# Performance work log

Hardware: AMD Instinct MI355X
Metric: run time of the kernel (lower is better)

Reference implementation:

```python
import jax, jax.numpy as jnp
import numpy as np

N_NODES = 50000
N_EDGES = 800000
D_MODEL = 128
N_HEADS = 8
HEAD_DIM = D_MODEL // N_HEADS
EPS = 1e-5


def setup_inputs() -> dict:
    key = jax.random.key(0)
    ks = jax.random.split(key, 8)
    return {
        "node_feature": jax.random.normal(ks[0], (N_NODES, D_MODEL), jnp.float32),
        "dist_attn": jax.random.normal(ks[1], (N_EDGES, N_HEADS), jnp.float32),
        "path_attn": jax.random.normal(ks[2], (N_EDGES, N_HEADS), jnp.float32),
        "gamma": jnp.ones((D_MODEL,), jnp.float32),
        "beta": jnp.zeros((D_MODEL,), jnp.float32),
        "W_qkv": jax.random.normal(ks[3], (3 * D_MODEL, D_MODEL), jnp.float32) * (D_MODEL ** -0.5),
        "b_qkv": jnp.zeros((3 * D_MODEL,), jnp.float32),
        "W_out": jax.random.normal(ks[4], (D_MODEL, D_MODEL), jnp.float32) * (D_MODEL ** -0.5),
        "b_out": jnp.zeros((D_MODEL,), jnp.float32),
        "src": jax.random.randint(ks[5], (N_EDGES,), 0, N_NODES, jnp.int32),
        "dst": jax.random.randint(ks[6], (N_EDGES,), 0, N_NODES, jnp.int32),
    }


def reference(node_feature, dist_attn, path_attn, gamma, beta,
              W_qkv, b_qkv, W_out, b_out, src, dst):
    res = node_feature
    # LayerNorm
    mu = jnp.mean(node_feature, axis=-1, keepdims=True)
    var = jnp.var(node_feature, axis=-1, keepdims=True)
    x = (node_feature - mu) * jax.lax.rsqrt(var + EPS) * gamma + beta
    # QKV projection; scale = d_model**-0.5 (as in source, full d_model)
    qkv = (x @ W_qkv.T + b_qkv).reshape(-1, 3, N_HEADS, HEAD_DIM)
    q = qkv[:, 0] * (D_MODEL ** -0.5)  # [N, H, Dh]
    k = qkv[:, 1]
    v = qkv[:, 2]
    # u_dot_v: dot of src Q with dst K per edge/head -> [E, H]
    node_attn = jnp.einsum("ehd,ehd->eh", q[src], k[dst])
    a = node_attn + dist_attn + path_attn  # [E, H]
    # edge_softmax: segmented softmax over incoming edges of each dst node
    m = jax.ops.segment_max(a, dst, num_segments=N_NODES)  # [N, H]
    ex = jnp.exp(a - m[dst])
    denom = jax.ops.segment_sum(ex, dst, num_segments=N_NODES)  # [N, H]
    sa = ex / denom[dst]  # [E, H]
    # weighted message from src v, summed into dst
    he = v[src] * sa[:, :, None]  # [E, H, Dh]
    agg = jax.ops.segment_sum(he, dst, num_segments=N_NODES)  # [N, H, Dh]
    agg = agg.reshape(-1, D_MODEL)
    out = res + (agg @ W_out.T + b_out)
    return out
```

## Files before the change

kernel.cpp:

```cpp
#include <hip/hip_runtime.h>
#include <math.h>

#define N_NODES 50000
#define N_EDGES 800000
#define D 128
#define NH 8
#define EPS 1e-5f
#define QSCALE 0.08838834764831845f

#define TQ 24
#define TO 8

typedef __attribute__((ext_vector_type(8))) short short8;
typedef __attribute__((ext_vector_type(4))) float f32x4;

__device__ __forceinline__ unsigned short f2bf_rne(float f) {
    unsigned int u = __float_as_uint(f);
    u += 0x7fff + ((u >> 16) & 1);
    return (unsigned short)(u >> 16);
}
__device__ __forceinline__ float bf2f(unsigned short h) {
    return __uint_as_float(((unsigned int)h) << 16);
}
__device__ __forceinline__ float2 bfpair(unsigned int u) {
    return make_float2(__uint_as_float(u << 16),
                       __uint_as_float(u & 0xffff0000u));
}

__device__ __forceinline__ void gload_lds16(const void* g, void* l) {
    __builtin_amdgcn_global_load_lds(
        (const __attribute__((address_space(1))) unsigned int*)g,
        (__attribute__((address_space(3))) unsigned int*)l, 16, 0, 0);
}

__device__ __forceinline__ float qdot(uint4 u, float4 kv) {
    float2 q0 = bfpair(u.x), q1 = bfpair(u.z);
    return q0.x * kv.x + q0.y * kv.y + q1.x * kv.z + q1.y * kv.w;
}
__device__ __forceinline__ void vacc(uint4 u, float w, float& sden,
                                     float& a0, float& a1, float& a2, float& a3) {
    float2 v0 = bfpair(u.y), v1 = bfpair(u.w);
    sden += w;
    a0 += w * v0.x; a1 += w * v0.y; a2 += w * v1.x; a3 += w * v1.y;
}

__global__ void k_prep(const float* __restrict__ Wqkv, const float* __restrict__ Wout,
                       unsigned short* __restrict__ wq_t, unsigned short* __restrict__ wo_t,
                       int* __restrict__ cnt) {
    const int i = blockIdx.x * blockDim.x + threadIdx.x;
    if (i < N_NODES) cnt[i] = 0;
    if (i < TQ * 256) {
        const int nt = i >> 8, r = (i >> 4) & 15, c8 = i & 15;
        const float* s = Wqkv + (size_t)(nt * 16 + r) * D + c8 * 8;
        short8 h8, l8;
        #pragma unroll
        for (int j = 0; j < 8; j++) {
            float w = s[j];
            unsigned short h = f2bf_rne(w);
            h8[j] = (short)h;
            l8[j] = (short)f2bf_rne(w - bf2f(h));
        }
        const int off = (r * 256 + c8 * 16) ^ ((r & 7) << 4);
        char* base = (char*)wq_t + (size_t)nt * 8192;
        *(short8*)(base + off)        = h8;
        *(short8*)(base + 4096 + off) = l8;
    }
    if (i < TO * 256) {
        const int nt = i >> 8, r = (i >> 4) & 15, c8 = i & 15;
        const float* s = Wout + (size_t)(nt * 16 + r) * D + c8 * 8;
        short8 h8, l8;
        #pragma unroll
        for (int j = 0; j < 8; j++) {
            float w = s[j];
            unsigned short h = f2bf_rne(w);
            h8[j] = (short)h;
            l8[j] = (short)f2bf_rne(w - bf2f(h));
        }
        const int off = (r * 256 + c8 * 16) ^ ((r & 7) << 4);
        char* base = (char*)wo_t + (size_t)nt * 8192;
        *(short8*)(base + off)        = h8;
        *(short8*)(base + 4096 + off) = l8;
    }
}

__global__ void k_hist(const int* __restrict__ dst, int* __restrict__ cnt,
                       int* __restrict__ rank) {
    const int e0 = (blockIdx.x * blockDim.x + threadIdx.x) * 4;
    if (e0 >= N_EDGES) return;
    const int4 d4 = *(const int4*)(dst + e0);
    int r0 = atomicAdd(&cnt[d4.x], 1);
    int r1 = atomicAdd(&cnt[d4.y], 1);
    int r2 = atomicAdd(&cnt[d4.z], 1);
    int r3 = atomicAdd(&cnt[d4.w], 1);
    *(int4*)(rank + e0) = make_int4(r0, r1, r2, r3);
}

#define SCB 1024
#define SCG ((N_NODES + SCB - 1) / SCB)

__global__ void k_scan1(const int* __restrict__ cnt, int* __restrict__ row_start,
                        int* __restrict__ bsum) {
    __shared__ int wsum[16];
    const int tid = threadIdx.x, lane = tid & 63, wid = tid >> 6;
    const int gid = blockIdx.x * SCB + tid;
    const int v = (gid < N_NODES) ? cnt[gid] : 0;

    int x = v;
    #pragma unroll
    for (int off = 1; off < 64; off <<= 1) {
        int t = __shfl_up(x, off);
        if (lane >= off) x += t;
    }
    if (lane == 63) wsum[wid] = x;
    __syncthreads();
    if (wid == 0) {
        int w = (lane < 16) ? wsum[lane] : 0;
        #pragma unroll
        for (int off = 1; off < 16; off <<= 1) {
            int t = __shfl_up(w, off);
            if (lane >= off) w += t;
        }
        if (lane < 16) wsum[lane] = w;
    }
    __syncthreads();
    const int base = (wid > 0) ? wsum[wid - 1] : 0;
    const int incl = base + x;
    if (gid < N_NODES) row_start[gid] = incl - v;
    if (tid == SCB - 1) bsum[blockIdx.x] = incl;
}

__global__ void k_scan2(const int* __restrict__ bsum, int* __restrict__ row_start) {
    __shared__ int boff_s;
    const int tid = threadIdx.x;
    if (tid < 64) {
        int v = (tid < blockIdx.x) ? bsum[tid] : 0;
        #pragma unroll
        for (int off = 1; off < 64; off <<= 1) v += __shfl_xor(v, off);
        if (tid == 0) boff_s = v;
    }
    __syncthreads();
    const int gid = blockIdx.x * SCB + tid;
    if (gid < N_NODES) row_start[gid] += boff_s;
    if (gid == 0) row_start[N_NODES] = N_EDGES;
}

__global__ void k_fill(const int* __restrict__ src, const int* __restrict__ dst,
                       const int* __restrict__ rank, const int* __restrict__ row_start,
                       const float* __restrict__ dist, const float* __restrict__ path,
                       int* __restrict__ ssrc, unsigned short* __restrict__ dp16) {
    const int e0 = (blockIdx.x * blockDim.x + threadIdx.x) * 4;
    if (e0 >= N_EDGES) return;
    const int4 s4 = *(const int4*)(src + e0);
    const int4 d4 = *(const int4*)(dst + e0);
    const int4 r4 = *(const int4*)(rank + e0);
    int p0 = row_start[d4.x] + r4.x;
    int p1 = row_start[d4.y] + r4.y;
    int p2 = row_start[d4.z] + r4.z;
    int p3 = row_start[d4.w] + r4.w;

    const int ss[4] = {s4.x, s4.y, s4.z, s4.w};
    const int pp[4] = {p0, p1, p2, p3};
    #pragma unroll
    for (int j = 0; j < 4; j++) {
        const int e = e0 + j;
        float4 da = *(const float4*)(dist + (size_t)e * 8);
        float4 db = *(const float4*)(dist + (size_t)e * 8 + 4);
        float4 pa = *(const float4*)(path + (size_t)e * 8);
        float4 pb = *(const float4*)(path + (size_t)e * 8 + 4);
        short8 w;
        w[0] = (short)f2bf_rne(da.x + pa.x);
        w[1] = (short)f2bf_rne(da.y + pa.y);
        w[2] = (short)f2bf_rne(da.z + pa.z);
        w[3] = (short)f2bf_rne(da.w + pa.w);
        w[4] = (short)f2bf_rne(db.x + pb.x);
        w[5] = (short)f2bf_rne(db.y + pb.y);
        w[6] = (short)f2bf_rne(db.z + pb.z);
        w[7] = (short)f2bf_rne(db.w + pb.w);
        ssrc[pp[j]] = ss[j];
        *(short8*)(dp16 + (size_t)pp[j] * 8) = w;
    }
}

__launch_bounds__(256)
__global__ void k_ln_qkv(const float* __restrict__ nf, const float* __restrict__ gamma,
                         const float* __restrict__ beta,
                         const unsigned short* __restrict__ wq_t,
                         const float* __restrict__ bqkv,
                         unsigned short* __restrict__ qv, float* __restrict__ kb) {
    __shared__ __align__(16) char lds[2][8192];
    const int lane  = threadIdx.x & 63;
    const int wv    = threadIdx.x >> 6;
    const int nbase = blockIdx.x * 64 + wv * 16;
    const int mrow  = lane & 15;
    const int kg    = lane >> 4;

    int gn = nbase + mrow;
    if (gn >= N_NODES) gn = N_NODES - 1;
    const float* xrow = nf + (size_t)gn * D + kg * 8;
    float4 xa[4], xb[4];
    #pragma unroll
    for (int t = 0; t < 4; t++) {
        xa[t] = *(const float4*)(xrow + t * 32);
        xb[t] = *(const float4*)(xrow + t * 32 + 4);
    }
    float s = 0.f, ss = 0.f;
    #pragma unroll
    for (int t = 0; t < 4; t++) {
        s  += xa[t].x + xa[t].y + xa[t].z + xa[t].w
            + xb[t].x + xb[t].y + xb[t].z + xb[t].w;
        ss += xa[t].x * xa[t].x + xa[t].y * xa[t].y + xa[t].z * xa[t].z + xa[t].w * xa[t].w
            + xb[t].x * xb[t].x + xb[t].y * xb[t].y + xb[t].z * xb[t].z + xb[t].w * xb[t].w;
    }
    s += __shfl_xor(s, 16); ss += __shfl_xor(ss, 16);
    s += __shfl_xor(s, 32); ss += __shfl_xor(ss, 32);
    float mu   = s * (1.f / 128.f);
    float var  = ss * (1.f / 128.f) - mu * mu;
    float rstd = rsqrtf(var + EPS);

    short8 ahi[4], alo[4];
    #pragma unroll
    for (int t = 0; t < 4; t++) {
        const float* gp = gamma + kg * 8 + t * 32;
        const float* bp = beta  + kg * 8 + t * 32;
        float4 g0 = *(const float4*)gp, g1 = *(const float4*)(gp + 4);
        float4 b0 = *(const float4*)bp, b1 = *(const float4*)(bp + 4);
        float xn[8];
        xn[0] = (xa[t].x - mu) * rstd * g0.x + b0.x;
        xn[1] = (xa[t].y - mu) * rstd * g0.y + b0.y;
        xn[2] = (xa[t].z - mu) * rstd * g0.z + b0.z;
        xn[3] = (xa[t].w - mu) * rstd * g0.w + b0.w;
        xn[4] = (xb[t].x - mu) * rstd * g1.x + b1.x;
        xn[5] = (xb[t].y - mu) * rstd * g1.y + b1.y;
        xn[6] = (xb[t].z - mu) * rstd * g1.z + b1.z;
        xn[7] = (xb[t].w - mu) * rstd * g1.w + b1.w;
        #pragma unroll
        for (int j = 0; j < 8; j++) {
            unsigned short h = f2bf_rne(xn[j]);
            ahi[t][j] = (short)h;
            alo[t][j] = (short)f2bf_rne(xn[j] - bf2f(h));
        }
    }

    int boff[4];
    #pragma unroll
    for (int t = 0; t < 4; t++)
        boff[t] = (mrow * 256 + (kg + 4 * t) * 16) ^ ((mrow & 7) << 4);

    {
        const char* g0 = (const char*)wq_t + (size_t)0 * 8192 + wv * 2048 + lane * 16;
        gload_lds16(g0,        lds[0] + wv * 2048);
        gload_lds16(g0 + 1024, lds[0] + wv * 2048 + 1024);
    }
    __syncthreads();

    int cur = 0;
    for (int nt = 0; nt < TQ; ++nt) {
        if (nt + 1 < TQ) {
            const char* g0 = (const char*)wq_t + (size_t)(nt + 1) * 8192 + wv * 2048 + lane * 16;
            gload_lds16(g0,        lds[cur ^ 1] + wv * 2048);
            gload_lds16(g0 + 1024, lds[cur ^ 1] + wv * 2048 + 1024);
        }

        f32x4 acc0 = {0.f, 0.f, 0.f, 0.f};
        f32x4 acc1 = {0.f, 0.f, 0.f, 0.f};
        #pragma unroll
        for (int t = 0; t < 4; t++) {
            short8 bh = *(const short8*)(lds[cur] + boff[t]);
            short8 bl = *(const short8*)(lds[cur] + 4096 + boff[t]);
            acc0 = __builtin_amdgcn_mfma_f32_16x16x32_bf16(ahi[t], bh, acc0, 0, 0, 0);
            acc1 = __builtin_amdgcn_mfma_f32_16x16x32_bf16(alo[t], bh, acc1, 0, 0, 0);
            acc0 = __builtin_amdgcn_mfma_f32_16x16x32_bf16(ahi[t], bl, acc0, 0, 0, 0);
        }

        const int col = nt * 16 + mrow;
        if (nt < 8) {
            float bias = bqkv[col];
            #pragma unroll
            for (int r = 0; r < 4; r++) {
                int node = nbase + kg * 4 + r;
                unsigned int hq = f2bf_rne((acc0[r] + acc1[r] + bias) * QSCALE);
                unsigned int ph = __shfl_xor((int)hq, 1);
                if (!(mrow & 1) && node < N_NODES) {
                    unsigned int u2 = (hq & 0xffffu) | (ph << 16);
                    *(unsigned int*)(qv + (size_t)node * 256 + ((col >> 1) << 2)) = u2;
                }
            }
        } else if (nt < 16) {
            float bias = bqkv[col];
            #pragma unroll
            for (int r = 0; r < 4; r++) {
                int node = nbase + kg * 4 + r;
                if (node < N_NODES)
                    kb[(size_t)node * D + (col - 128)] = acc0[r] + acc1[r] + bias;
            }
        } else {
            float bias = bqkv[col];
            #pragma unroll
            for (int r = 0; r < 4; r++) {
                int node = nbase + kg * 4 + r;
                unsigned int hq = f2bf_rne(acc0[r] + acc1[r] + bias);
                unsigned int ph = __shfl_xor((int)hq, 1);
                if (!(mrow & 1) && node < N_NODES) {
                    unsigned int u2 = (hq & 0xffffu) | (ph << 16);
                    int cv = col - 256;
                    *(unsigned int*)(qv + (size_t)node * 256 + ((cv >> 1) << 2) + 2) = u2;
                }
            }
        }

        __syncthreads();
        cur ^= 1;
    }
}

__launch_bounds__(256, 4)
__global__ void k_gather(const unsigned short* __restrict__ qv,
                         const float* __restrict__ kb,
                         const unsigned short* __restrict__ dp16,
                         const int* __restrict__ row_start,
                         const int* __restrict__ ssrc,
                         float* __restrict__ agg) {
    const int node = blockIdx.x * 4 + (threadIdx.x >> 6);
    if (node >= N_NODES) return;
    const int lane = threadIdx.x & 63;
    const int half = lane >> 5;
    const int l    = lane & 31;
    const int h    = l >> 2;
    const int beg = row_start[node], end = row_start[node + 1];

    const float4 kv = *(const float4*)(kb + (size_t)node * D + 4 * l);
    float sden = 0.f, a0 = 0.f, a1 = 0.f, a2 = 0.f, a3 = 0.f;

    int i = beg + half;
    for (; i + 6 < end; i += 8) {
        int s0 = ssrc[i], s1 = ssrc[i + 2], s2 = ssrc[i + 4], s3 = ssrc[i + 6];
        uint4 u0 = *(const uint4*)(qv + (size_t)s0 * 256 + l * 8);
        uint4 u1 = *(const uint4*)(qv + (size_t)s1 * 256 + l * 8);
        uint4 u2 = *(const uint4*)(qv + (size_t)s2 * 256 + l * 8);
        uint4 u3 = *(const uint4*)(qv + (size_t)s3 * 256 + l * 8);
        float d0 = bf2f(dp16[(size_t)i * 8 + h]);
        float d1 = bf2f(dp16[(size_t)(i + 2) * 8 + h]);
        float d2 = bf2f(dp16[(size_t)(i + 4) * 8 + h]);
        float d3 = bf2f(dp16[(size_t)(i + 6) * 8 + h]);

        float p0 = qdot(u0, kv), p1 = qdot(u1, kv);
        float p2 = qdot(u2, kv), p3 = qdot(u3, kv);
        p0 += __shfl_xor(p0, 1); p1 += __shfl_xor(p1, 1);
        p2 += __shfl_xor(p2, 1); p3 += __shfl_xor(p3, 1);
        p0 += __shfl_xor(p0, 2); p1 += __shfl_xor(p1, 2);
        p2 += __shfl_xor(p2, 2); p3 += __shfl_xor(p3, 2);

        float w0 = __expf(p0 + d0), w1 = __expf(p1 + d1);
        float w2 = __expf(p2 + d2), w3 = __expf(p3 + d3);
        vacc(u0, w0, sden, a0, a1, a2, a3);
        vacc(u1, w1, sden, a0, a1, a2, a3);
        vacc(u2, w2, sden, a0, a1, a2, a3);
        vacc(u3, w3, sden, a0, a1, a2, a3);
    }
    if (i + 2 < end) {
        int s0 = ssrc[i], s1 = ssrc[i + 2];
        uint4 u0 = *(const uint4*)(qv + (size_t)s0 * 256 + l * 8);
        uint4 u1 = *(const uint4*)(qv + (size_t)s1 * 256 + l * 8);
        float d0 = bf2f(dp16[(size_t)i * 8 + h]);
        float d1 = bf2f(dp16[(size_t)(i + 2) * 8 + h]);
        float p0 = qdot(u0, kv), p1 = qdot(u1, kv);
        p0 += __shfl_xor(p0, 1); p1 += __shfl_xor(p1, 1);
        p0 += __shfl_xor(p0, 2); p1 += __shfl_xor(p1, 2);
        float w0 = __expf(p0 + d0), w1 = __expf(p1 + d1);
        vacc(u0, w0, sden, a0, a1, a2, a3);
        vacc(u1, w1, sden, a0, a1, a2, a3);
        i += 4;
    }
    if (i < end) {
        int s0 = ssrc[i];
        uint4 u0 = *(const uint4*)(qv + (size_t)s0 * 256 + l * 8);
        float d0 = bf2f(dp16[(size_t)i * 8 + h]);
        float p0 = qdot(u0, kv);
        p0 += __shfl_xor(p0, 1); p0 += __shfl_xor(p0, 2);
        float w0 = __expf(p0 + d0);
        vacc(u0, w0, sden, a0, a1, a2, a3);
    }

    sden += __shfl_xor(sden, 32);
    a0 += __shfl_xor(a0, 32);
    a1 += __shfl_xor(a1, 32);
    a2 += __shfl_xor(a2, 32);
    a3 += __shfl_xor(a3, 32);

    const float inv = (end > beg) ? 1.f / sden : 0.f;
    if (half == 0) {
        float4 r = make_float4(a0 * inv, a1 * inv, a2 * inv, a3 * inv);
        *(float4*)(agg + (size_t)node * D + 4 * l) = r;
    }
}

__launch_bounds__(256)
__global__ void k_out(const float* __restrict__ agg,
                      const unsigned short* __restrict__ wo_t,
                      const float* __restrict__ bout, const float* __restrict__ nf,
                      float* __restrict__ out) {
    __shared__ __align__(16) char lds[2][8192];
    const int lane  = threadIdx.x & 63;
    const int wv    = threadIdx.x >> 6;
    const int nbase = blockIdx.x * 64 + wv * 16;
    const int mrow  = lane & 15;
    const int kg    = lane >> 4;

    int gn = nbase + mrow;
    if (gn >= N_NODES) gn = N_NODES - 1;
    const float* arow = agg + (size_t)gn * D + kg * 8;

    short8 ahi[4], alo[4];
    #pragma unroll
    for (int t = 0; t < 4; t++) {
        float4 x0 = *(const float4*)(arow + t * 32);
        float4 x1 = *(const float4*)(arow + t * 32 + 4);
        float xn[8] = {x0.x, x0.y, x0.z, x0.w, x1.x, x1.y, x1.z, x1.w};
        #pragma unroll
        for (int j = 0; j < 8; j++) {
            unsigned short h = f2bf_rne(xn[j]);
            ahi[t][j] = (short)h;
            alo[t][j] = (short)f2bf_rne(xn[j] - bf2f(h));
        }
    }

    int boff[4];
    #pragma unroll
    for (int t = 0; t < 4; t++)
        boff[t] = (mrow * 256 + (kg + 4 * t) * 16) ^ ((mrow & 7) << 4);

    {
        const char* g0 = (const char*)wo_t + (size_t)0 * 8192 + wv * 2048 + lane * 16;
        gload_lds16(g0,        lds[0] + wv * 2048);
        gload_lds16(g0 + 1024, lds[0] + wv * 2048 + 1024);
    }
    __syncthreads();

    int cur = 0;
    for (int nt = 0; nt < TO; ++nt) {
        if (nt + 1 < TO) {
            const char* g0 = (const char*)wo_t + (size_t)(nt + 1) * 8192 + wv * 2048 + lane * 16;
            gload_lds16(g0,        lds[cur ^ 1] + wv * 2048);
            gload_lds16(g0 + 1024, lds[cur ^ 1] + wv * 2048 + 1024);
        }

        f32x4 acc0 = {0.f, 0.f, 0.f, 0.f};
        f32x4 acc1 = {0.f, 0.f, 0.f, 0.f};
        #pragma unroll
        for (int t = 0; t < 4; t++) {
            short8 bh = *(const short8*)(lds[cur] + boff[t]);
            short8 bl = *(const short8*)(lds[cur] + 4096 + boff[t]);
            acc0 = __builtin_amdgcn_mfma_f32_16x16x32_bf16(ahi[t], bh, acc0, 0, 0, 0);
            acc1 = __builtin_amdgcn_mfma_f32_16x16x32_bf16(alo[t], bh, acc1, 0, 0, 0);
            acc0 = __builtin_amdgcn_mfma_f32_16x16x32_bf16(ahi[t], bl, acc0, 0, 0, 0);
        }

        const int col = nt * 16 + mrow;
        float bias = bout[col];
        #pragma unroll
        for (int r = 0; r < 4; r++) {
            int node = nbase + kg * 4 + r;
            if (node < N_NODES)
                out[(size_t)node * D + col] =
                    nf[(size_t)node * D + col] + bias + acc0[r] + acc1[r];
        }

        __syncthreads();
        cur ^= 1;
    }
}

extern "C" void kernel_launch(void* const* d_in, const int* in_sizes, int n_in,
                              void* d_out, int out_size, void* d_ws, size_t ws_size,
                              hipStream_t stream) {
    const float* nf    = (const float*)d_in[0];
    const float* dist  = (const float*)d_in[1];
    const float* path  = (const float*)d_in[2];
    const float* gamma = (const float*)d_in[3];
    const float* beta  = (const float*)d_in[4];
    const float* Wqkv  = (const float*)d_in[5];
    const float* bqkv  = (const float*)d_in[6];
    const float* Wout  = (const float*)d_in[7];
    const float* bout  = (const float*)d_in[8];
    const int*   src   = (const int*)d_in[9];
    const int*   dst   = (const int*)d_in[10];
    float* out = (float*)d_out;

    float* kb  = (float*)d_ws;
    float* agg = kb + (size_t)N_NODES * D;
    unsigned short* qvb  = (unsigned short*)(agg + (size_t)N_NODES * D);
    unsigned short* dp16 = qvb + (size_t)N_NODES * 256;
    int* ssrc      = (int*)(dp16 + (size_t)N_EDGES * 8);
    int* rank      = ssrc + N_EDGES;
    int* cnt       = rank + N_EDGES;
    int* row_start = cnt + N_NODES;
    int* bsum      = row_start + N_NODES + 1;
    uintptr_t p = (uintptr_t)(bsum + 64);
    p = (p + 15) & ~(uintptr_t)15;
    unsigned short* wq_t = (unsigned short*)p;
    unsigned short* wo_t = wq_t + TQ * 4096;

    (void)in_sizes; (void)n_in; (void)out_size; (void)ws_size;

    hipLaunchKernelGGL(k_prep, dim3((N_NODES + 255) / 256), dim3(256), 0, stream,
                       Wqkv, Wout, wq_t, wo_t, cnt);

    hipLaunchKernelGGL(k_hist, dim3((N_EDGES / 4 + 255) / 256), dim3(256), 0, stream,
                       dst, cnt, rank);
    hipLaunchKernelGGL(k_scan1, dim3(SCG), dim3(SCB), 0, stream,
                       cnt, row_start, bsum);
    hipLaunchKernelGGL(k_scan2, dim3(SCG), dim3(SCB), 0, stream,
                       bsum, row_start);
    hipLaunchKernelGGL(k_fill, dim3((N_EDGES / 4 + 255) / 256), dim3(256), 0, stream,
                       src, dst, rank, row_start, dist, path, ssrc, dp16);

    hipLaunchKernelGGL(k_ln_qkv, dim3((N_NODES + 63) / 64), dim3(256), 0, stream,
                       nf, gamma, beta, wq_t, bqkv, qvb, kb);

    hipLaunchKernelGGL(k_gather, dim3((N_NODES + 3) / 4), dim3(256), 0, stream,
                       qvb, kb, dp16, row_start, ssrc, agg);

    hipLaunchKernelGGL(k_out, dim3((N_NODES + 63) / 64), dim3(256), 0, stream,
                       agg, wo_t, bout, nf, out);
}
```

Baseline: 204.2 us.

## Precombine dist+path in hist pass and store K as bf16

The bf16 conversion of dist+path moves from the scatter kernel into the histogram kernel, which now writes it in edge order. The fill kernel then only copies 16-byte packed rows to their CSR positions instead of reading 64 bytes of fp32 per edge at scatter time. K is stored as bf16 instead of fp32, halving its footprint and its read in the gather kernel. This adds an extra intermediate buffer with a write and read, and the lower K precision may cost accuracy.

```diff
diff --git a/kernel.cpp b/kernel.cpp
--- a/kernel.cpp
+++ b/kernel.cpp
@@ -83,8 +83,10 @@
     }
 }
 
-__global__ void k_hist(const int* __restrict__ dst, int* __restrict__ cnt,
-                       int* __restrict__ rank) {
+__global__ void k_hist(const int* __restrict__ dst,
+                       const float* __restrict__ dist, const float* __restrict__ path,
+                       int* __restrict__ cnt, int* __restrict__ rank,
+                       unsigned short* __restrict__ dps) {
     const int e0 = (blockIdx.x * blockDim.x + threadIdx.x) * 4;
     if (e0 >= N_EDGES) return;
     const int4 d4 = *(const int4*)(dst + e0);
@@ -92,74 +94,6 @@
     int r1 = atomicAdd(&cnt[d4.y], 1);
     int r2 = atomicAdd(&cnt[d4.z], 1);
     int r3 = atomicAdd(&cnt[d4.w], 1);
-    *(int4*)(rank + e0) = make_int4(r0, r1, r2, r3);
-}
-
-#define SCB 1024
-#define SCG ((N_NODES + SCB - 1) / SCB)
-
-__global__ void k_scan1(const int* __restrict__ cnt, int* __restrict__ row_start,
-                        int* __restrict__ bsum) {
-    __shared__ int wsum[16];
-    const int tid = threadIdx.x, lane = tid & 63, wid = tid >> 6;
-    const int gid = blockIdx.x * SCB + tid;
-    const int v = (gid < N_NODES) ? cnt[gid] : 0;
-
-    int x = v;
-    #pragma unroll
-    for (int off = 1; off < 64; off <<= 1) {
-        int t = __shfl_up(x, off);
-        if (lane >= off) x += t;
-    }
-    if (lane == 63) wsum[wid] = x;
-    __syncthreads();
-    if (wid == 0) {
-        int w = (lane < 16) ? wsum[lane] : 0;
-        #pragma unroll
-        for (int off = 1; off < 16; off <<= 1) {
-            int t = __shfl_up(w, off);
-            if (lane >= off) w += t;
-        }
-        if (lane < 16) wsum[lane] = w;
-    }
-    __syncthreads();
-    const int base = (wid > 0) ? wsum[wid - 1] : 0;
-    const int incl = base + x;
-    if (gid < N_NODES) row_start[gid] = incl - v;
-    if (tid == SCB - 1) bsum[blockIdx.x] = incl;
-}
-
-__global__ void k_scan2(const int* __restrict__ bsum, int* __restrict__ row_start) {
-    __shared__ int boff_s;
-    const int tid = threadIdx.x;
-    if (tid < 64) {
-        int v = (tid < blockIdx.x) ? bsum[tid] : 0;
-        #pragma unroll
-        for (int off = 1; off < 64; off <<= 1) v += __shfl_xor(v, off);
-        if (tid == 0) boff_s = v;
-    }
-    __syncthreads();
-    const int gid = blockIdx.x * SCB + tid;
-    if (gid < N_NODES) row_start[gid] += boff_s;
-    if (gid == 0) row_start[N_NODES] = N_EDGES;
-}
-
-__global__ void k_fill(const int* __restrict__ src, const int* __restrict__ dst,
-                       const int* __restrict__ rank, const int* __restrict__ row_start,
-                       const float* __restrict__ dist, const float* __restrict__ path,
-                       int* __restrict__ ssrc, unsigned short* __restrict__ dp16) {
-    const int e0 = (blockIdx.x * blockDim.x + threadIdx.x) * 4;
-    if (e0 >= N_EDGES) return;
-    const int4 s4 = *(const int4*)(src + e0);
-    const int4 d4 = *(const int4*)(dst + e0);
-    const int4 r4 = *(const int4*)(rank + e0);
-    int p0 = row_start[d4.x] + r4.x;
-    int p1 = row_start[d4.y] + r4.y;
-    int p2 = row_start[d4.z] + r4.z;
-    int p3 = row_start[d4.w] + r4.w;
-
-    const int ss[4] = {s4.x, s4.y, s4.z, s4.w};
-    const int pp[4] = {p0, p1, p2, p3};
     #pragma unroll
     for (int j = 0; j < 4; j++) {
         const int e = e0 + j;
@@ -176,9 +110,82 @@
         w[5] = (short)f2bf_rne(db.y + pb.y);
         w[6] = (short)f2bf_rne(db.z + pb.z);
         w[7] = (short)f2bf_rne(db.w + pb.w);
-        ssrc[pp[j]] = ss[j];
-        *(short8*)(dp16 + (size_t)pp[j] * 8) = w;
-    }
+        *(short8*)(dps + (size_t)e * 8) = w;
+    }
+    *(int4*)(rank + e0) = make_int4(r0, r1, r2, r3);
+}
+
+#define SCB 1024
+#define SCG ((N_NODES + SCB - 1) / SCB)
+
+__global__ void k_scan1(const int* __restrict__ cnt, int* __restrict__ row_start,
+                        int* __restrict__ bsum) {
+    __shared__ int wsum[16];
+    const int tid = threadIdx.x, lane = tid & 63, wid = tid >> 6;
+    const int gid = blockIdx.x * SCB + tid;
+    const int v = (gid < N_NODES) ? cnt[gid] : 0;
+
+    int x = v;
+    #pragma unroll
+    for (int off = 1; off < 64; off <<= 1) {
+        int t = __shfl_up(x, off);
+        if (lane >= off) x += t;
+    }
+    if (lane == 63) wsum[wid] = x;
+    __syncthreads();
+    if (wid == 0) {
+        int w = (lane < 16) ? wsum[lane] : 0;
+        #pragma unroll
+        for (int off = 1; off < 16; off <<= 1) {
+            int t = __shfl_up(w, off);
+            if (lane >= off) w += t;
+        }
+        if (lane < 16) wsum[lane] = w;
+    }
+    __syncthreads();
+    const int base = (wid > 0) ? wsum[wid - 1] : 0;
+    const int incl = base + x;
+    if (gid < N_NODES) row_start[gid] = incl - v;
+    if (tid == SCB - 1) bsum[blockIdx.x] = incl;
+}
+
+__global__ void k_scan2(const int* __restrict__ bsum, int* __restrict__ row_start) {
+    __shared__ int boff_s;
+    const int tid = threadIdx.x;
+    if (tid < 64) {
+        int v = (tid < blockIdx.x) ? bsum[tid] : 0;
+        #pragma unroll
+        for (int off = 1; off < 64; off <<= 1) v += __shfl_xor(v, off);
+        if (tid == 0) boff_s = v;
+    }
+    __syncthreads();
+    const int gid = blockIdx.x * SCB + tid;
+    if (gid < N_NODES) row_start[gid] += boff_s;
+    if (gid == 0) row_start[N_NODES] = N_EDGES;
+}
+
+__global__ void k_fill(const int* __restrict__ src, const int* __restrict__ dst,
+                       const int* __restrict__ rank, const int* __restrict__ row_start,
+                       const unsigned short* __restrict__ dps,
+                       int* __restrict__ ssrc, unsigned short* __restrict__ dp16) {
+    const int e0 = (blockIdx.x * blockDim.x + threadIdx.x) * 4;
+    if (e0 >= N_EDGES) return;
+    const int4 s4 = *(const int4*)(src + e0);
+    const int4 d4 = *(const int4*)(dst + e0);
+    const int4 r4 = *(const int4*)(rank + e0);
+    int p0 = row_start[d4.x] + r4.x;
+    int p1 = row_start[d4.y] + r4.y;
+    int p2 = row_start[d4.z] + r4.z;
+    int p3 = row_start[d4.w] + r4.w;
+    short8 w0 = *(const short8*)(dps + (size_t)e0 * 8);
+    short8 w1 = *(const short8*)(dps + (size_t)(e0 + 1) * 8);
+    short8 w2 = *(const short8*)(dps + (size_t)(e0 + 2) * 8);
+    short8 w3 = *(const short8*)(dps + (size_t)(e0 + 3) * 8);
+
+    ssrc[p0] = s4.x;  *(short8*)(dp16 + (size_t)p0 * 8) = w0;
+    ssrc[p1] = s4.y;  *(short8*)(dp16 + (size_t)p1 * 8) = w1;
+    ssrc[p2] = s4.z;  *(short8*)(dp16 + (size_t)p2 * 8) = w2;
+    ssrc[p3] = s4.w;  *(short8*)(dp16 + (size_t)p3 * 8) = w3;
 }
 
 __launch_bounds__(256)
@@ -186,7 +193,8 @@
                          const float* __restrict__ beta,
                          const unsigned short* __restrict__ wq_t,
                          const float* __restrict__ bqkv,
-                         unsigned short* __restrict__ qv, float* __restrict__ kb) {
+                         unsigned short* __restrict__ qv,
+                         unsigned short* __restrict__ kb16) {
     __shared__ __align__(16) char lds[2][8192];
     const int lane  = threadIdx.x & 63;
     const int wv    = threadIdx.x >> 6;
@@ -273,8 +281,8 @@
         }
 
         const int col = nt * 16 + mrow;
+        float bias = bqkv[col];
         if (nt < 8) {
-            float bias = bqkv[col];
             #pragma unroll
             for (int r = 0; r < 4; r++) {
                 int node = nbase + kg * 4 + r;
@@ -286,15 +294,18 @@
                 }
             }
         } else if (nt < 16) {
-            float bias = bqkv[col];
             #pragma unroll
             for (int r = 0; r < 4; r++) {
                 int node = nbase + kg * 4 + r;
-                if (node < N_NODES)
-                    kb[(size_t)node * D + (col - 128)] = acc0[r] + acc1[r] + bias;
+                unsigned int hq = f2bf_rne(acc0[r] + acc1[r] + bias);
+                unsigned int ph = __shfl_xor((int)hq, 1);
+                if (!(mrow & 1) && node < N_NODES) {
+                    unsigned int u2 = (hq & 0xffffu) | (ph << 16);
+                    int ck = col - 128;
+                    *(unsigned int*)(kb16 + (size_t)node * 128 + (ck & ~1)) = u2;
+                }
             }
         } else {
-            float bias = bqkv[col];
             #pragma unroll
             for (int r = 0; r < 4; r++) {
                 int node = nbase + kg * 4 + r;
@@ -315,7 +326,7 @@
 
 __launch_bounds__(256, 4)
 __global__ void k_gather(const unsigned short* __restrict__ qv,
-                         const float* __restrict__ kb,
+                         const unsigned short* __restrict__ kb16,
                          const unsigned short* __restrict__ dp16,
                          const int* __restrict__ row_start,
                          const int* __restrict__ ssrc,
@@ -328,7 +339,9 @@
     const int h    = l >> 2;
     const int beg = row_start[node], end = row_start[node + 1];
 
-    const float4 kv = *(const float4*)(kb + (size_t)node * D + 4 * l);
+    uint2 ku = *(const uint2*)(kb16 + (size_t)node * 128 + 4 * l);
+    float2 k0 = bfpair(ku.x), k1 = bfpair(ku.y);
+    const float4 kv = make_float4(k0.x, k0.y, k1.x, k1.y);
     float sden = 0.f, a0 = 0.f, a1 = 0.f, a2 = 0.f, a3 = 0.f;
 
     int i = beg + half;
@@ -486,10 +499,11 @@
     const int*   dst   = (const int*)d_in[10];
     float* out = (float*)d_out;
 
-    float* kb  = (float*)d_ws;
-    float* agg = kb + (size_t)N_NODES * D;
+    float* agg = (float*)d_ws;
     unsigned short* qvb  = (unsigned short*)(agg + (size_t)N_NODES * D);
-    unsigned short* dp16 = qvb + (size_t)N_NODES * 256;
+    unsigned short* kb16 = qvb + (size_t)N_NODES * 256;
+    unsigned short* dps  = kb16 + (size_t)N_NODES * 128;
+    unsigned short* dp16 = dps + (size_t)N_EDGES * 8;
     int* ssrc      = (int*)(dp16 + (size_t)N_EDGES * 8);
     int* rank      = ssrc + N_EDGES;
     int* cnt       = rank + N_EDGES;
@@ -506,19 +520,19 @@
                        Wqkv, Wout, wq_t, wo_t, cnt);
 
     hipLaunchKernelGGL(k_hist, dim3((N_EDGES / 4 + 255) / 256), dim3(256), 0, stream,
-                       dst, cnt, rank);
+                       dst, dist, path, cnt, rank, dps);
     hipLaunchKernelGGL(k_scan1, dim3(SCG), dim3(SCB), 0, stream,
                        cnt, row_start, bsum);
     hipLaunchKernelGGL(k_scan2, dim3(SCG), dim3(SCB), 0, stream,
                        bsum, row_start);
     hipLaunchKernelGGL(k_fill, dim3((N_EDGES / 4 + 255) / 256), dim3(256), 0, stream,
-                       src, dst, rank, row_start, dist, path, ssrc, dp16);
+                       src, dst, rank, row_start, dps, ssrc, dp16);
 
     hipLaunchKernelGGL(k_ln_qkv, dim3((N_NODES + 63) / 64), dim3(256), 0, stream,
-                       nf, gamma, beta, wq_t, bqkv, qvb, kb);
+                       nf, gamma, beta, wq_t, bqkv, qvb, kb16);
 
     hipLaunchKernelGGL(k_gather, dim3((N_NODES + 3) / 4), dim3(256), 0, stream,
-                       qvb, kb, dp16, row_start, ssrc, agg);
+                       qvb, kb16, dp16, row_start, ssrc, agg);
 
     hipLaunchKernelGGL(k_out, dim3((N_NODES + 63) / 64), dim3(256), 0, stream,
                        agg, wo_t, bout, nf, out);
```

After: 195.4 us (median of 2 runs). 1.04x faster.
